# Optimization experiments

Measured on AMD Instinct MI355X. Metric: run time of the kernel, lower is better.

The kernel has to match this reference:

```python
import jax, jax.numpy as jnp
import numpy as np

B, L, D, H, DK, DV = 2, 2048, 512, 8, 64, 64
EPS = 1e-6


def setup_inputs() -> dict:
    key = jax.random.key(0)
    ks = jax.random.split(key, 19)
    n = lambda k, s: jax.random.normal(k, s, dtype=jnp.float32)
    inp = {
        "q_r": n(ks[0], (B, L, D)), "q_i": n(ks[1], (B, L, D)),
        "k_r": n(ks[2], (B, L, D)), "k_i": n(ks[3], (B, L, D)),
        "v_r": n(ks[4], (B, L, D)), "v_i": n(ks[5], (B, L, D)),
        "wq_r": n(ks[6], (D, H * DK)) * 0.02, "wq_i": n(ks[7], (D, H * DK)) * 0.02,
        "wk_r": n(ks[8], (D, H * DK)) * 0.02, "wk_i": n(ks[9], (D, H * DK)) * 0.02,
        "wv_r": n(ks[10], (D, H * DV)) * 0.02, "wv_i": n(ks[11], (D, H * DV)) * 0.02,
        "wo_r": n(ks[12], (H * DV, D)) * 0.02, "wo_i": n(ks[13], (H * DV, D)) * 0.02,
        "ln_wr": n(ks[14], (D,)), "ln_wi": n(ks[15], (D,)),
        "ln_br": n(ks[16], (D,)), "ln_bi": n(ks[17], (D,)),
        "mask": jax.random.randint(ks[18], (B, L, L), 0, 2).astype(jnp.int32),
    }
    return inp


def _clinear(xr, xi, wr, wi):
    # complex matmul (xr + i xi) @ (wr + i wi)
    return xr @ wr - xi @ wi, xi @ wr + xr @ wi


def _complex_layernorm(r, i, wr, wi, br, bi, eps=EPS):
    axes = (1, 2)  # normalize over all non-batch dims of [B, L, D]
    r = r - r.mean(axis=axes, keepdims=True)
    i = i - i.mean(axis=axes, keepdims=True)
    Crr = (r * r).mean(axis=axes, keepdims=True) + eps
    Cii = (i * i).mean(axis=axes, keepdims=True) + eps
    Cri = (r * i).mean(axis=axes, keepdims=True)
    s = jnp.sqrt(Crr * Cii - Cri * Cri)
    t = jnp.sqrt(Crr + Cii + 2.0 * s)
    inv_st = 1.0 / (s * t)
    Rrr = (Cii + s) * inv_st
    Rii = (Crr + s) * inv_st
    Rri = -Cri * inv_st
    nr = Rrr * r + Rri * i
    ni = Rii * i + Rri * r
    # affine: complex multiply by (wr + i wi), then add complex bias
    out_r = nr * wr - ni * wi + br
    out_i = nr * wi + ni * wr + bi
    return out_r, out_i


def reference(q_r, q_i, k_r, k_i, v_r, v_i,
              wq_r, wq_i, wk_r, wk_i, wv_r, wv_i, wo_r, wo_i,
              ln_wr, ln_wi, ln_br, ln_bi, mask):
    res_r, res_i = q_r, q_i
    qr, qi = _clinear(q_r, q_i, wq_r, wq_i)
    kr, ki = _clinear(k_r, k_i, wk_r, wk_i)
    vr, vi = _clinear(v_r, v_i, wv_r, wv_i)
    # [B, L, H*Dk] -> [B, H, L, Dk]
    tohead = lambda x, d: x.reshape(B, L, H, d).transpose(0, 2, 1, 3)
    qr, qi = tohead(qr, DK), tohead(qi, DK)
    kr, ki = tohead(kr, DK), tohead(ki, DK)
    vr, vi = tohead(vr, DV), tohead(vi, DV)
    temp = jnp.float32(DK) ** 0.5
    qr, qi = qr / temp, qi / temp
    # complex scores (q @ conj(k)^T): re + i*im
    sr = jnp.einsum('bhqd,bhkd->bhqk', qr, kr) + jnp.einsum('bhqd,bhkd->bhqk', qi, ki)
    si = jnp.einsum('bhqd,bhkd->bhqk', qi, kr) - jnp.einsum('bhqd,bhkd->bhqk', qr, ki)
    a = jnp.sqrt(sr * sr + si * si)  # abs of complex scores
    a = jnp.where(mask[:, None, :, :] == 0, jnp.float32(-1e9), a)
    attn = jax.nn.softmax(a, axis=-1)  # real-valued attention weights
    out_r = jnp.einsum('bhqk,bhkd->bhqd', attn, vr)
    out_i = jnp.einsum('bhqk,bhkd->bhqd', attn, vi)
    # [B, H, L, Dv] -> [B, L, H*Dv]
    out_r = out_r.transpose(0, 2, 1, 3).reshape(B, L, H * DV)
    out_i = out_i.transpose(0, 2, 1, 3).reshape(B, L, H * DV)
    out_r, out_i = _clinear(out_r, out_i, wo_r, wo_i)
    out_r = out_r + res_r
    out_i = out_i + res_i
    out_r, out_i = _complex_layernorm(out_r, out_i, ln_wr, ln_wi, ln_br, ln_bi)
    return out_r, out_i, attn
```

## Files before the change

kernel.cpp:

```cpp
#include <hip/hip_runtime.h>

typedef unsigned short u16;
typedef unsigned int u32;
typedef unsigned long long u64;


typedef __attribute__((ext_vector_type(8))) short bf16x8;
typedef __attribute__((ext_vector_type(4))) float f32x4;
typedef __attribute__((ext_vector_type(4))) u32 u32x4;

__device__ __forceinline__ u16 f2bf(float f) {
  u32 x = __float_as_uint(f);
  return (u16)((x + 0x7FFFu + ((x >> 16) & 1u)) >> 16);
}
__device__ __forceinline__ u32 pk2(float a, float b) {
  return (u32)f2bf(a) | ((u32)f2bf(b) << 16);
}
__device__ __forceinline__ bf16x8 negv(bf16x8 v) {
  u32x4 x = __builtin_bit_cast(u32x4, v);
  x ^= 0x80008000u;
  return __builtin_bit_cast(bf16x8, x);
}


__global__ __launch_bounds__(256) void pack_a3(
    const float* __restrict__ qr, const float* __restrict__ qi,
    const float* __restrict__ kr, const float* __restrict__ ki,
    const float* __restrict__ vr, const float* __restrict__ vi,
    u16* __restrict__ A) {
  int z = blockIdx.y;
  const float* r  = (z == 0) ? qr : (z == 1) ? kr : vr;
  const float* im = (z == 0) ? qi : (z == 1) ? ki : vi;
  int c = blockIdx.x * 256 + threadIdx.x;
  int m = c >> 7;
  int ck = (c & 127) * 8;
  const float* s = (ck < 512) ? (r + (size_t)m * 512 + ck)
                              : (im + (size_t)m * 512 + (ck - 512));
  float4 a = ((const float4*)s)[0];
  float4 b = ((const float4*)s)[1];
  uint4 o;
  o.x = pk2(a.x, a.y); o.y = pk2(a.z, a.w);
  o.z = pk2(b.x, b.y); o.w = pk2(b.z, b.w);
  ((uint4*)(A + (size_t)z * 4194304))[c] = o;
}

__global__ __launch_bounds__(256) void pack_bt(
    const float* __restrict__ wqr, const float* __restrict__ wqi,
    const float* __restrict__ wkr, const float* __restrict__ wki,
    const float* __restrict__ wvr, const float* __restrict__ wvi,
    const float* __restrict__ wor, const float* __restrict__ woi,
    u16* __restrict__ Btb) {
  int z = blockIdx.y;
  const float* wr = (z==0)?wqr:(z==1)?wkr:(z==2)?wvr:wor;
  const float* wi = (z==0)?wqi:(z==1)?wki:(z==2)?wvi:woi;
  u16* Bt = Btb + (size_t)z * 1048576;
  int n0 = (blockIdx.x >> 4) * 64;
  int k0 = (blockIdx.x & 15) * 64;
  __shared__ float tile[64][65];
  int t = threadIdx.x;
  bool nlow = (n0 < 512), klow = (k0 < 512);
  const float* src = nlow ? (klow ? wr : wi) : (klow ? wi : wr);
  float sgn = (nlow && !klow) ? -1.0f : 1.0f;
  int col0 = nlow ? n0 : n0 - 512;
  int kr0 = klow ? k0 : k0 - 512;
  {
    int rr = t >> 2, cc = (t & 3) * 16;
    const float4* s = (const float4*)(src + (size_t)(kr0 + rr) * 512 + col0 + cc);
#pragma unroll
    for (int j = 0; j < 4; ++j) {
      float4 v = s[j];
      tile[rr][cc + j*4 + 0] = v.x; tile[rr][cc + j*4 + 1] = v.y;
      tile[rr][cc + j*4 + 2] = v.z; tile[rr][cc + j*4 + 3] = v.w;
    }
  }
  __syncthreads();
  {
    int nn = t >> 2, kc = (t & 3) * 16;
    u32 w[8];
#pragma unroll
    for (int j = 0; j < 8; ++j)
      w[j] = pk2(sgn * tile[kc + 2*j][nn], sgn * tile[kc + 2*j + 1][nn]);
    uint4* d = (uint4*)(Bt + (size_t)(n0 + nn) * 1024 + k0 + kc);
    d[0] = make_uint4(w[0], w[1], w[2], w[3]);
    d[1] = make_uint4(w[4], w[5], w[6], w[7]);
  }
}

__global__ __launch_bounds__(256) void pack_mask(const int* __restrict__ mask,
                                                 u64* __restrict__ mb) {
  int tid = blockIdx.x * 256 + threadIdx.x;
  u64 bal = __ballot(mask[tid] != 0);
  if ((threadIdx.x & 63) == 0) mb[tid >> 6] = bal;
}

__global__ __launch_bounds__(256) void pack_vt(const u16* __restrict__ Cvm,
                                               u16* __restrict__ vt) {
  int z = blockIdx.y;
  int b = z >> 3, h = z & 7;
  int lt = blockIdx.x >> 1, ct = blockIdx.x & 1;
  int l0 = lt * 64, c0 = ct * 64;
  int n0 = (ct == 0) ? (h * 64) : (512 + h * 64);
  __shared__ u16 tile[64][80];
  int t = threadIdx.x;
  {
    int lr = t >> 2, cc = (t & 3) * 16;
    const uint4* s = (const uint4*)(Cvm + ((size_t)(b * 2048 + l0 + lr)) * 1024 + n0 + cc);
    uint4 v0 = s[0], v1 = s[1];
    *(uint4*)&tile[lr][cc] = v0;
    *(uint4*)&tile[lr][cc + 8] = v1;
  }
  __syncthreads();
  {
    int cr = t >> 2, lc = (t & 3) * 16;
    u32 w[8];
#pragma unroll
    for (int j = 0; j < 8; ++j)
      w[j] = (u32)tile[lc + 2*j][cr] | ((u32)tile[lc + 2*j + 1][cr] << 16);
    uint4* d = (uint4*)(vt + ((size_t)z * 128 + c0 + cr) * 2048 + l0 + lc);
    d[0] = make_uint4(w[0], w[1], w[2], w[3]);
    d[1] = make_uint4(w[4], w[5], w[6], w[7]);
  }
}


__device__ __forceinline__ void stage_bf(const u16* __restrict__ g, int ld,
                                         u16* lds, int t) {
#pragma unroll
  for (int p = 0; p < 4; ++p) {
    int id = p * 256 + t;
    int r = id >> 3, c = id & 7;
    uint4 v = *(const uint4*)(g + (size_t)r * ld + c * 8);
    *(uint4*)(lds + r * 64 + ((c ^ (r & 7)) << 3)) = v;
  }
}
__device__ __forceinline__ void stage64(const u16* __restrict__ g, int ld,
                                        u16* lds, int t) {
#pragma unroll
  for (int p = 0; p < 2; ++p) {
    int id = p * 256 + t;
    int r = id >> 3, c = id & 7;
    uint4 v = *(const uint4*)(g + (size_t)r * ld + c * 8);
    *(uint4*)(lds + r * 64 + ((c ^ (r & 7)) << 3)) = v;
  }
}

__global__ __launch_bounds__(256) void gemm_proj(const u16* __restrict__ Abase,
                                                 const u16* __restrict__ Btbase,
                                                 u16* __restrict__ Cbase) {
  __shared__ u16 lA[128 * 64], lB[128 * 64];
  int t = threadIdx.x, lane = t & 63, wid = t >> 6;
  int c15 = lane & 15, g = lane >> 4, l7 = lane & 7;
  int z = blockIdx.z;
  const u16* A  = Abase  + (size_t)z * 4194304;
  const u16* Bt = Btbase + (size_t)z * 1048576;
  u16* C = Cbase + (size_t)z * 4194304;
  int brow = blockIdx.y * 128, bcol = blockIdx.x * 128;
  float scale = (z == 0) ? 0.125f : 1.0f;
  int sw0 = ((g ^ l7) << 3), sw1 = (((4 | g) ^ l7) << 3);
  int wr0 = (wid >> 1) * 64 + c15, wc0 = (wid & 1) * 64 + c15;
  const u16 *pA0 = lA + wr0 * 64 + sw0, *pA1 = lA + wr0 * 64 + sw1;
  const u16 *pB0 = lB + wc0 * 64 + sw0, *pB1 = lB + wc0 * 64 + sw1;
  f32x4 zero = {0.f, 0.f, 0.f, 0.f};
  f32x4 acc[4][4];
#pragma unroll
  for (int mi = 0; mi < 4; ++mi)
#pragma unroll
    for (int ni = 0; ni < 4; ++ni) acc[mi][ni] = zero;
  for (int kt = 0; kt < 1024; kt += 64) {
    stage_bf(A + (size_t)brow * 1024 + kt, 1024, lA, t);
    stage_bf(Bt + (size_t)bcol * 1024 + kt, 1024, lB, t);
    __syncthreads();
#pragma unroll
    for (int ks = 0; ks < 2; ++ks) {
      const u16* pa = ks ? pA1 : pA0;
      const u16* pb = ks ? pB1 : pB0;
      bf16x8 fa[4], fb[4];
#pragma unroll
      for (int i2 = 0; i2 < 4; ++i2) {
        fa[i2] = *(const bf16x8*)(pa + i2 * 1024);
        fb[i2] = *(const bf16x8*)(pb + i2 * 1024);
      }
#pragma unroll
      for (int mi = 0; mi < 4; ++mi)
#pragma unroll
        for (int ni = 0; ni < 4; ++ni)
          acc[mi][ni] = __builtin_amdgcn_mfma_f32_16x16x32_bf16(
              fa[mi], fb[ni], acc[mi][ni], 0, 0, 0);
    }
    __syncthreads();
  }
  int wrb = (wid >> 1) * 64, wcb = (wid & 1) * 64;
  int rj = g * 4, cj = c15;
#pragma unroll
  for (int mi = 0; mi < 4; ++mi)
#pragma unroll
    for (int ni = 0; ni < 4; ++ni)
#pragma unroll
      for (int j = 0; j < 4; ++j)
        C[(size_t)(brow + wrb + mi * 16 + rj + j) * 1024 +
          (bcol + wcb + ni * 16 + cj)] = f2bf(acc[mi][ni][j] * scale);
}

__global__ __launch_bounds__(256, 3) void fused_attn(
    const u16* __restrict__ Cq, const u16* __restrict__ Ck,
    const u16* __restrict__ vt, const u64* __restrict__ mb,
    float* __restrict__ attn, u16* __restrict__ Ao) {
  __shared__ u16 lKr[64 * 64], lKi[64 * 64], lV[128 * 64], lP[64 * 64];
  int t = threadIdx.x, lane = t & 63, w = t >> 6;
  int c15 = lane & 15, g = lane >> 4, l7 = lane & 7;
  int strip = blockIdx.x, z = blockIdx.y;
  int b = z >> 3, h = z & 7;
  int q0 = strip * 64;
  int arow = w * 16 + c15;
  int rbase = w * 16 + (g << 2);

  const u16* Qrow = Cq + ((size_t)(b * 2048 + q0 + arow)) * 1024 + h * 64;
  bf16x8 q0r = *(const bf16x8*)(Qrow + g * 8);
  bf16x8 q1r = *(const bf16x8*)(Qrow + 32 + g * 8);
  bf16x8 q0i = *(const bf16x8*)(Qrow + 512 + g * 8);
  bf16x8 q1i = *(const bf16x8*)(Qrow + 544 + g * 8);
  bf16x8 nq0r = negv(q0r), nq1r = negv(q1r);

  int sw0 = ((g ^ l7) << 3), sw1 = (((4 | g) ^ l7) << 3);
  const u16 *pKr0 = lKr + c15 * 64 + sw0, *pKr1 = lKr + c15 * 64 + sw1;
  const u16 *pKi0 = lKi + c15 * 64 + sw0, *pKi1 = lKi + c15 * 64 + sw1;
  const u16 *pV0 = lV + c15 * 64 + sw0, *pV1 = lV + c15 * 64 + sw1;
  const u16 *pP0 = lP + arow * 64 + sw0, *pP1 = lP + arow * 64 + sw1;

  size_t mbase = ((size_t)(b * 2048 + q0 + rbase)) * 32;
  float s[4] = {0.f, 0.f, 0.f, 0.f};
  f32x4 zero = {0.f, 0.f, 0.f, 0.f};
  f32x4 o[8];
#pragma unroll
  for (int ni = 0; ni < 8; ++ni) o[ni] = zero;

  const u16* Kb = Ck + ((size_t)(b * 2048)) * 1024 + h * 64;
  const u16* Vb = vt + (size_t)z * 262144;

  for (int tl = 0; tl < 32; ++tl) {
    int l0 = tl * 64;
    if (tl) __syncthreads();
    stage64(Kb + (size_t)l0 * 1024, 1024, lKr, t);
    stage64(Kb + (size_t)l0 * 1024 + 512, 1024, lKi, t);
    stage_bf(Vb + l0, 2048, lV, t);
    __syncthreads();
    f32x4 sr[4], si[4];
#pragma unroll
    for (int ni = 0; ni < 4; ++ni) { sr[ni] = zero; si[ni] = zero; }
#pragma unroll
    for (int ni = 0; ni < 4; ++ni) {
      bf16x8 g0 = *(const bf16x8*)(pKr0 + ni * 1024);
      bf16x8 g1 = *(const bf16x8*)(pKi0 + ni * 1024);
      sr[ni] = __builtin_amdgcn_mfma_f32_16x16x32_bf16(q0r, g0, sr[ni], 0, 0, 0);
      sr[ni] = __builtin_amdgcn_mfma_f32_16x16x32_bf16(q0i, g1, sr[ni], 0, 0, 0);
      si[ni] = __builtin_amdgcn_mfma_f32_16x16x32_bf16(q0i, g0, si[ni], 0, 0, 0);
      si[ni] = __builtin_amdgcn_mfma_f32_16x16x32_bf16(nq0r, g1, si[ni], 0, 0, 0);
      bf16x8 h0 = *(const bf16x8*)(pKr1 + ni * 1024);
      bf16x8 h1 = *(const bf16x8*)(pKi1 + ni * 1024);
      sr[ni] = __builtin_amdgcn_mfma_f32_16x16x32_bf16(q1r, h0, sr[ni], 0, 0, 0);
      sr[ni] = __builtin_amdgcn_mfma_f32_16x16x32_bf16(q1i, h1, sr[ni], 0, 0, 0);
      si[ni] = __builtin_amdgcn_mfma_f32_16x16x32_bf16(q1i, h0, si[ni], 0, 0, 0);
      si[ni] = __builtin_amdgcn_mfma_f32_16x16x32_bf16(nq1r, h1, si[ni], 0, 0, 0);
    }
    u64 wm[4];
#pragma unroll
    for (int j = 0; j < 4; ++j) wm[j] = mb[mbase + (size_t)j * 32 + tl];
#pragma unroll
    for (int ni = 0; ni < 4; ++ni) {
      int cbit = ni * 16 + c15;
      int pchi = ni * 2 + (c15 >> 3);
#pragma unroll
      for (int j = 0; j < 4; ++j) {
        float n = sr[ni][j] * sr[ni][j] + si[ni][j] * si[ni][j];
        float p = __expf(__builtin_amdgcn_sqrtf(n));
        p = ((wm[j] >> cbit) & 1ull) ? p : 0.0f;
        s[j] += p;
        lP[(rbase + j) * 64 + ((pchi ^ (((g & 1) << 2) + j)) << 3) + l7] = f2bf(p);
      }
    }
    {
      bf16x8 fa0 = *(const bf16x8*)pP0;
      bf16x8 fa1 = *(const bf16x8*)pP1;
#pragma unroll
      for (int ni = 0; ni < 8; ++ni) {
        bf16x8 fb0 = *(const bf16x8*)(pV0 + ni * 1024);
        bf16x8 fb1 = *(const bf16x8*)(pV1 + ni * 1024);
        o[ni] = __builtin_amdgcn_mfma_f32_16x16x32_bf16(fa0, fb0, o[ni], 0, 0, 0);
        o[ni] = __builtin_amdgcn_mfma_f32_16x16x32_bf16(fa1, fb1, o[ni], 0, 0, 0);
      }
    }
  }
  float inv[4];
#pragma unroll
  for (int j = 0; j < 4; ++j) {
    float sj = s[j];
#pragma unroll
    for (int off = 1; off < 16; off <<= 1) sj += __shfl_xor(sj, off);
    inv[j] = 1.0f / sj;
  }
#pragma unroll
  for (int ni = 0; ni < 8; ++ni) {
    int c = ni * 16 + c15;
    int nout = (c < 64) ? (h * 64 + c) : (512 + h * 64 + (c - 64));
#pragma unroll
    for (int j = 0; j < 4; ++j)
      Ao[((size_t)(b * 2048 + q0 + rbase + j)) * 1024 + nout] =
          f2bf(o[ni][j] * inv[j]);
  }
  float* arow_out = attn + ((size_t)z * 2048 + q0 + rbase) * 2048 + c15;
  for (int tl = 0; tl < 32; ++tl) {
    int l0 = tl * 64;
    __syncthreads();
    stage64(Kb + (size_t)l0 * 1024, 1024, lKr, t);
    stage64(Kb + (size_t)l0 * 1024 + 512, 1024, lKi, t);
    __syncthreads();
    f32x4 sr[4], si[4];
#pragma unroll
    for (int ni = 0; ni < 4; ++ni) { sr[ni] = zero; si[ni] = zero; }
#pragma unroll
    for (int ni = 0; ni < 4; ++ni) {
      bf16x8 g0 = *(const bf16x8*)(pKr0 + ni * 1024);
      bf16x8 g1 = *(const bf16x8*)(pKi0 + ni * 1024);
      sr[ni] = __builtin_amdgcn_mfma_f32_16x16x32_bf16(q0r, g0, sr[ni], 0, 0, 0);
      sr[ni] = __builtin_amdgcn_mfma_f32_16x16x32_bf16(q0i, g1, sr[ni], 0, 0, 0);
      si[ni] = __builtin_amdgcn_mfma_f32_16x16x32_bf16(q0i, g0, si[ni], 0, 0, 0);
      si[ni] = __builtin_amdgcn_mfma_f32_16x16x32_bf16(nq0r, g1, si[ni], 0, 0, 0);
      bf16x8 h0 = *(const bf16x8*)(pKr1 + ni * 1024);
      bf16x8 h1 = *(const bf16x8*)(pKi1 + ni * 1024);
      sr[ni] = __builtin_amdgcn_mfma_f32_16x16x32_bf16(q1r, h0, sr[ni], 0, 0, 0);
      sr[ni] = __builtin_amdgcn_mfma_f32_16x16x32_bf16(q1i, h1, sr[ni], 0, 0, 0);
      si[ni] = __builtin_amdgcn_mfma_f32_16x16x32_bf16(q1i, h0, si[ni], 0, 0, 0);
      si[ni] = __builtin_amdgcn_mfma_f32_16x16x32_bf16(nq1r, h1, si[ni], 0, 0, 0);
    }
    u64 wm[4];
#pragma unroll
    for (int j = 0; j < 4; ++j) wm[j] = mb[mbase + (size_t)j * 32 + tl];
    float* outp = arow_out + l0;
#pragma unroll
    for (int ni = 0; ni < 4; ++ni) {
      int cbit = ni * 16 + c15;
#pragma unroll
      for (int j = 0; j < 4; ++j) {
        float n = sr[ni][j] * sr[ni][j] + si[ni][j] * si[ni][j];
        float p = __expf(__builtin_amdgcn_sqrtf(n)) * inv[j];
        p = ((wm[j] >> cbit) & 1ull) ? p : 0.0f;
        outp[(size_t)j * 2048 + ni * 16] = p;
      }
    }
  }
}

__global__ __launch_bounds__(256) void gemm_oproj(
    const u16* __restrict__ A, const u16* __restrict__ Bt,
    const float* __restrict__ resR, const float* __restrict__ resI,
    float* __restrict__ outR, float* __restrict__ outI) {
  __shared__ u16 lA[128 * 64], lB[128 * 64];
  int t = threadIdx.x, lane = t & 63, wid = t >> 6;
  int c15 = lane & 15, g = lane >> 4, l7 = lane & 7;
  int brow = blockIdx.y * 128, bcol = blockIdx.x * 128;
  int sw0 = ((g ^ l7) << 3), sw1 = (((4 | g) ^ l7) << 3);
  int wr0 = (wid >> 1) * 64 + c15, wc0 = (wid & 1) * 64 + c15;
  const u16 *pA0 = lA + wr0 * 64 + sw0, *pA1 = lA + wr0 * 64 + sw1;
  const u16 *pB0 = lB + wc0 * 64 + sw0, *pB1 = lB + wc0 * 64 + sw1;
  f32x4 zero = {0.f, 0.f, 0.f, 0.f};
  f32x4 acc[4][4];
#pragma unroll
  for (int mi = 0; mi < 4; ++mi)
#pragma unroll
    for (int ni = 0; ni < 4; ++ni) acc[mi][ni] = zero;
  for (int kt = 0; kt < 1024; kt += 64) {
    stage_bf(A + (size_t)brow * 1024 + kt, 1024, lA, t);
    stage_bf(Bt + (size_t)bcol * 1024 + kt, 1024, lB, t);
    __syncthreads();
#pragma unroll
    for (int ks = 0; ks < 2; ++ks) {
      const u16* pa = ks ? pA1 : pA0;
      const u16* pb = ks ? pB1 : pB0;
      bf16x8 fa[4], fb[4];
#pragma unroll
      for (int i2 = 0; i2 < 4; ++i2) {
        fa[i2] = *(const bf16x8*)(pa + i2 * 1024);
        fb[i2] = *(const bf16x8*)(pb + i2 * 1024);
      }
#pragma unroll
      for (int mi = 0; mi < 4; ++mi)
#pragma unroll
        for (int ni = 0; ni < 4; ++ni)
          acc[mi][ni] = __builtin_amdgcn_mfma_f32_16x16x32_bf16(
              fa[mi], fb[ni], acc[mi][ni], 0, 0, 0);
    }
    __syncthreads();
  }
  int wrb = (wid >> 1) * 64, wcb = (wid & 1) * 64;
  int rj = g * 4, cj = c15;
#pragma unroll
  for (int mi = 0; mi < 4; ++mi)
#pragma unroll
    for (int ni = 0; ni < 4; ++ni)
#pragma unroll
      for (int j = 0; j < 4; ++j) {
        int row = brow + wrb + mi * 16 + rj + j;
        int col = bcol + wcb + ni * 16 + cj;
        float v = acc[mi][ni][j];
        if (col < 512)
          outR[(size_t)row * 512 + col] = v + resR[(size_t)row * 512 + col];
        else {
          int c2 = col - 512;
          outI[(size_t)row * 512 + c2] = v + resI[(size_t)row * 512 + c2];
        }
      }
}

__global__ __launch_bounds__(256) void ln_reduce(const float* __restrict__ outR,
                                                 const float* __restrict__ outI,
                                                 float* __restrict__ stats) {
  int b = blockIdx.y;
  int t = threadIdx.x;
  size_t base = (size_t)b * 1048576 + (size_t)blockIdx.x * 2048;
  float s0 = 0.f, s1 = 0.f, s2 = 0.f, s3 = 0.f, s4 = 0.f;
#pragma unroll
  for (int p = 0; p < 8; ++p) {
    size_t e = base + p * 256 + t;
    float r = outR[e], i = outI[e];
    s0 += r; s1 += i; s2 += r * r; s3 += i * i; s4 += r * i;
  }
#pragma unroll
  for (int off = 32; off; off >>= 1) {
    s0 += __shfl_xor(s0, off); s1 += __shfl_xor(s1, off);
    s2 += __shfl_xor(s2, off); s3 += __shfl_xor(s3, off);
    s4 += __shfl_xor(s4, off);
  }
  __shared__ float red[4][5];
  if ((t & 63) == 0) {
    int w = t >> 6;
    red[w][0] = s0; red[w][1] = s1; red[w][2] = s2; red[w][3] = s3; red[w][4] = s4;
  }
  __syncthreads();
  if (t == 0) {
    float a0 = red[0][0] + red[1][0] + red[2][0] + red[3][0];
    float a1 = red[0][1] + red[1][1] + red[2][1] + red[3][1];
    float a2 = red[0][2] + red[1][2] + red[2][2] + red[3][2];
    float a3 = red[0][3] + red[1][3] + red[2][3] + red[3][3];
    float a4 = red[0][4] + red[1][4] + red[2][4] + red[3][4];
    atomicAdd(&stats[b * 8 + 0], a0);
    atomicAdd(&stats[b * 8 + 1], a1);
    atomicAdd(&stats[b * 8 + 2], a2);
    atomicAdd(&stats[b * 8 + 3], a3);
    atomicAdd(&stats[b * 8 + 4], a4);
  }
}

__global__ __launch_bounds__(256) void ln_apply(
    float* __restrict__ outR, float* __restrict__ outI,
    const float* __restrict__ stats,
    const float* __restrict__ lnwr, const float* __restrict__ lnwi,
    const float* __restrict__ lnbr, const float* __restrict__ lnbi) {
  int b = blockIdx.y;
  const float* st = stats + b * 8;
  float iN = 1.0f / 1048576.0f;
  float mr = st[0] * iN, mi = st[1] * iN;
  float Crr = st[2] * iN - mr * mr + 1e-6f;
  float Cii = st[3] * iN - mi * mi + 1e-6f;
  float Cri = st[4] * iN - mr * mi;
  float s = sqrtf(fmaxf(Crr * Cii - Cri * Cri, 0.f));
  float tt = sqrtf(Crr + Cii + 2.f * s);
  float inv = 1.0f / (s * tt);
  float Rrr = (Cii + s) * inv, Rii = (Crr + s) * inv, Rri = -Cri * inv;
  size_t e = ((size_t)blockIdx.x * 256 + threadIdx.x) * 4;
  size_t idx = (size_t)b * 1048576 + e;
  int d = (int)(e & 511);
  float4 r4 = *(float4*)(outR + idx);
  float4 i4 = *(float4*)(outI + idx);
  float4 wr = *(const float4*)(lnwr + d);
  float4 wi = *(const float4*)(lnwi + d);
  float4 br = *(const float4*)(lnbr + d);
  float4 bi = *(const float4*)(lnbi + d);
  float4 orr, oii;
#pragma unroll
  for (int j = 0; j < 4; ++j) {
    float r = ((&r4.x)[j]) - mr;
    float i = ((&i4.x)[j]) - mi;
    float nr = Rrr * r + Rri * i;
    float ni = Rii * i + Rri * r;
    (&orr.x)[j] = nr * (&wr.x)[j] - ni * (&wi.x)[j] + (&br.x)[j];
    (&oii.x)[j] = nr * (&wi.x)[j] + ni * (&wr.x)[j] + (&bi.x)[j];
  }
  *(float4*)(outR + idx) = orr;
  *(float4*)(outI + idx) = oii;
}

extern "C" void kernel_launch(void* const* d_in, const int* in_sizes, int n_in,
                              void* d_out, int out_size, void* d_ws, size_t ws_size,
                              hipStream_t stream) {
  const float* q_r = (const float*)d_in[0];
  const float* q_i = (const float*)d_in[1];
  const float* k_r = (const float*)d_in[2];
  const float* k_i = (const float*)d_in[3];
  const float* v_r = (const float*)d_in[4];
  const float* v_i = (const float*)d_in[5];
  const float* wq_r = (const float*)d_in[6];
  const float* wq_i = (const float*)d_in[7];
  const float* wk_r = (const float*)d_in[8];
  const float* wk_i = (const float*)d_in[9];
  const float* wv_r = (const float*)d_in[10];
  const float* wv_i = (const float*)d_in[11];
  const float* wo_r = (const float*)d_in[12];
  const float* wo_i = (const float*)d_in[13];
  const float* ln_wr = (const float*)d_in[14];
  const float* ln_wi = (const float*)d_in[15];
  const float* ln_br = (const float*)d_in[16];
  const float* ln_bi = (const float*)d_in[17];
  const int* mask = (const int*)d_in[18];

  float* outR = (float*)d_out;
  float* outI = outR + 2097152;
  float* attn = outR + 4194304;

  char* ws = (char*)d_ws;
  u16* Aq = (u16*)ws;
  u16* Bt = (u16*)(ws + 25165824);
  u16* Cq = (u16*)(ws + 33554432);
  u16* Ck = Cq + 4194304;
  u16* Cv = Cq + 8388608;
  u16* vt = Aq;
  u16* Ao = (u16*)(ws + 58720256);
  u64* mb = (u64*)(ws + 67108864);
  float* stats = (float*)(ws + 69206016);

  pack_a3<<<dim3(2048, 3), 256, 0, stream>>>(q_r, q_i, k_r, k_i, v_r, v_i, Aq);
  pack_bt<<<dim3(256, 4), 256, 0, stream>>>(wq_r, wq_i, wk_r, wk_i, wv_r, wv_i,
                                            wo_r, wo_i, Bt);
  pack_mask<<<dim3(32768), 256, 0, stream>>>(mask, mb);
  gemm_proj<<<dim3(8, 32, 3), 256, 0, stream>>>(Aq, Bt, Cq);
  pack_vt<<<dim3(64, 16), 256, 0, stream>>>(Cv, vt);
  fused_attn<<<dim3(32, 16), 256, 0, stream>>>(Cq, Ck, vt, mb, attn, Ao);
  gemm_oproj<<<dim3(8, 32), 256, 0, stream>>>(Ao, Bt + 3145728, q_r, q_i, outR, outI);
  hipMemsetAsync(stats, 0, 64, stream);
  ln_reduce<<<dim3(512, 2), 256, 0, stream>>>(outR, outI, stats);
  ln_apply<<<dim3(1024, 2), 256, 0, stream>>>(outR, outI, stats, ln_wr, ln_wi,
                                              ln_br, ln_bi);
}
```

Baseline: 364.9 us.

## Prefetch next tiles into registers and double-buffer LDS in GEMMs and attention

Both GEMM kernels now load the next K-slice into registers while computing on the current LDS tile, then write it to LDS after the compute. The attention kernel double-buffers the K/V LDS tiles in both passes so global loads overlap MFMA work. It also remaps blocks so consecutive blocks share a head and batch, uses nontemporal stores for the attention matrix, and replaces hipMemsetAsync with a tiny zeroing kernel. The cost is more LDS and registers, so attention occupancy is lowered from 3 to 2 blocks per CU.

```diff
diff --git a/kernel.cpp b/kernel.cpp
--- a/kernel.cpp
+++ b/kernel.cpp
@@ -123,24 +123,38 @@
 }
 
 
-__device__ __forceinline__ void stage_bf(const u16* __restrict__ g, int ld,
-                                         u16* lds, int t) {
+__device__ __forceinline__ void ld_t64(const u16* __restrict__ g, int ld, int t,
+                                       uint4 r[2]) {
+#pragma unroll
+  for (int p = 0; p < 2; ++p) {
+    int id = p * 256 + t;
+    int rr = id >> 3, c = id & 7;
+    r[p] = *(const uint4*)(g + (size_t)rr * ld + c * 8);
+  }
+}
+__device__ __forceinline__ void st_t64(u16* lds, int t, const uint4 r[2]) {
+#pragma unroll
+  for (int p = 0; p < 2; ++p) {
+    int id = p * 256 + t;
+    int rr = id >> 3, c = id & 7;
+    *(uint4*)(lds + rr * 64 + ((c ^ (rr & 7)) << 3)) = r[p];
+  }
+}
+__device__ __forceinline__ void ld_t128(const u16* __restrict__ g, int ld, int t,
+                                        uint4 r[4]) {
 #pragma unroll
   for (int p = 0; p < 4; ++p) {
     int id = p * 256 + t;
-    int r = id >> 3, c = id & 7;
-    uint4 v = *(const uint4*)(g + (size_t)r * ld + c * 8);
-    *(uint4*)(lds + r * 64 + ((c ^ (r & 7)) << 3)) = v;
-  }
-}
-__device__ __forceinline__ void stage64(const u16* __restrict__ g, int ld,
-                                        u16* lds, int t) {
-#pragma unroll
-  for (int p = 0; p < 2; ++p) {
+    int rr = id >> 3, c = id & 7;
+    r[p] = *(const uint4*)(g + (size_t)rr * ld + c * 8);
+  }
+}
+__device__ __forceinline__ void st_t128(u16* lds, int t, const uint4 r[4]) {
+#pragma unroll
+  for (int p = 0; p < 4; ++p) {
     int id = p * 256 + t;
-    int r = id >> 3, c = id & 7;
-    uint4 v = *(const uint4*)(g + (size_t)r * ld + c * 8);
-    *(uint4*)(lds + r * 64 + ((c ^ (r & 7)) << 3)) = v;
+    int rr = id >> 3, c = id & 7;
+    *(uint4*)(lds + rr * 64 + ((c ^ (rr & 7)) << 3)) = r[p];
   }
 }
 
@@ -166,10 +180,19 @@
   for (int mi = 0; mi < 4; ++mi)
 #pragma unroll
     for (int ni = 0; ni < 4; ++ni) acc[mi][ni] = zero;
-  for (int kt = 0; kt < 1024; kt += 64) {
-    stage_bf(A + (size_t)brow * 1024 + kt, 1024, lA, t);
-    stage_bf(Bt + (size_t)bcol * 1024 + kt, 1024, lB, t);
+  const u16* Ab = A + (size_t)brow * 1024;
+  const u16* Bb = Bt + (size_t)bcol * 1024;
+  uint4 ra[4], rb[4];
+  ld_t128(Ab, 1024, t, ra);
+  ld_t128(Bb, 1024, t, rb);
+  st_t128(lA, t, ra);
+  st_t128(lB, t, rb);
+  for (int kt = 0; kt < 16; ++kt) {
     __syncthreads();
+    if (kt < 15) {
+      ld_t128(Ab + (kt + 1) * 64, 1024, t, ra);
+      ld_t128(Bb + (kt + 1) * 64, 1024, t, rb);
+    }
 #pragma unroll
     for (int ks = 0; ks < 2; ++ks) {
       const u16* pa = ks ? pA1 : pA0;
@@ -188,6 +211,10 @@
               fa[mi], fb[ni], acc[mi][ni], 0, 0, 0);
     }
     __syncthreads();
+    if (kt < 15) {
+      st_t128(lA, t, ra);
+      st_t128(lB, t, rb);
+    }
   }
   int wrb = (wid >> 1) * 64, wcb = (wid & 1) * 64;
   int rj = g * 4, cj = c15;
@@ -201,14 +228,16 @@
           (bcol + wcb + ni * 16 + cj)] = f2bf(acc[mi][ni][j] * scale);
 }
 
-__global__ __launch_bounds__(256, 3) void fused_attn(
+__global__ __launch_bounds__(256, 2) void fused_attn(
     const u16* __restrict__ Cq, const u16* __restrict__ Ck,
     const u16* __restrict__ vt, const u64* __restrict__ mb,
     float* __restrict__ attn, u16* __restrict__ Ao) {
-  __shared__ u16 lKr[64 * 64], lKi[64 * 64], lV[128 * 64], lP[64 * 64];
+  __shared__ u16 lKr[2][4096], lKi[2][4096], lV[2][8192], lP[4096];
   int t = threadIdx.x, lane = t & 63, w = t >> 6;
   int c15 = lane & 15, g = lane >> 4, l7 = lane & 7;
-  int strip = blockIdx.x, z = blockIdx.y;
+  int f = blockIdx.x + (int)gridDim.x * blockIdx.y;
+  int wk = (f & 7) * 64 + (f >> 3);
+  int strip = wk & 31, z = wk >> 5;
   int b = z >> 3, h = z & 7;
   int q0 = strip * 64;
   int arow = w * 16 + c15;
@@ -222,9 +251,6 @@
   bf16x8 nq0r = negv(q0r), nq1r = negv(q1r);
 
   int sw0 = ((g ^ l7) << 3), sw1 = (((4 | g) ^ l7) << 3);
-  const u16 *pKr0 = lKr + c15 * 64 + sw0, *pKr1 = lKr + c15 * 64 + sw1;
-  const u16 *pKi0 = lKi + c15 * 64 + sw0, *pKi1 = lKi + c15 * 64 + sw1;
-  const u16 *pV0 = lV + c15 * 64 + sw0, *pV1 = lV + c15 * 64 + sw1;
   const u16 *pP0 = lP + arow * 64 + sw0, *pP1 = lP + arow * 64 + sw1;
 
   size_t mbase = ((size_t)(b * 2048 + q0 + rbase)) * 32;
@@ -237,26 +263,39 @@
   const u16* Kb = Ck + ((size_t)(b * 2048)) * 1024 + h * 64;
   const u16* Vb = vt + (size_t)z * 262144;
 
+  uint4 kr[2], ki[2], vv[4];
+  ld_t64(Kb, 1024, t, kr);
+  ld_t64(Kb + 512, 1024, t, ki);
+  ld_t128(Vb, 2048, t, vv);
+  st_t64(lKr[0], t, kr);
+  st_t64(lKi[0], t, ki);
+  st_t128(lV[0], t, vv);
+
   for (int tl = 0; tl < 32; ++tl) {
-    int l0 = tl * 64;
-    if (tl) __syncthreads();
-    stage64(Kb + (size_t)l0 * 1024, 1024, lKr, t);
-    stage64(Kb + (size_t)l0 * 1024 + 512, 1024, lKi, t);
-    stage_bf(Vb + l0, 2048, lV, t);
+    int cur = tl & 1;
     __syncthreads();
+    if (tl < 31) {
+      size_t l1 = (size_t)(tl + 1) * 64;
+      ld_t64(Kb + l1 * 1024, 1024, t, kr);
+      ld_t64(Kb + l1 * 1024 + 512, 1024, t, ki);
+      ld_t128(Vb + l1, 2048, t, vv);
+    }
+    const u16* bKr = lKr[cur] + c15 * 64;
+    const u16* bKi = lKi[cur] + c15 * 64;
+    const u16* bV  = lV[cur] + c15 * 64;
     f32x4 sr[4], si[4];
 #pragma unroll
     for (int ni = 0; ni < 4; ++ni) { sr[ni] = zero; si[ni] = zero; }
 #pragma unroll
     for (int ni = 0; ni < 4; ++ni) {
-      bf16x8 g0 = *(const bf16x8*)(pKr0 + ni * 1024);
-      bf16x8 g1 = *(const bf16x8*)(pKi0 + ni * 1024);
+      bf16x8 g0 = *(const bf16x8*)(bKr + ni * 1024 + sw0);
+      bf16x8 g1 = *(const bf16x8*)(bKi + ni * 1024 + sw0);
       sr[ni] = __builtin_amdgcn_mfma_f32_16x16x32_bf16(q0r, g0, sr[ni], 0, 0, 0);
       sr[ni] = __builtin_amdgcn_mfma_f32_16x16x32_bf16(q0i, g1, sr[ni], 0, 0, 0);
       si[ni] = __builtin_amdgcn_mfma_f32_16x16x32_bf16(q0i, g0, si[ni], 0, 0, 0);
       si[ni] = __builtin_amdgcn_mfma_f32_16x16x32_bf16(nq0r, g1, si[ni], 0, 0, 0);
-      bf16x8 h0 = *(const bf16x8*)(pKr1 + ni * 1024);
-      bf16x8 h1 = *(const bf16x8*)(pKi1 + ni * 1024);
+      bf16x8 h0 = *(const bf16x8*)(bKr + ni * 1024 + sw1);
+      bf16x8 h1 = *(const bf16x8*)(bKi + ni * 1024 + sw1);
       sr[ni] = __builtin_amdgcn_mfma_f32_16x16x32_bf16(q1r, h0, sr[ni], 0, 0, 0);
       sr[ni] = __builtin_amdgcn_mfma_f32_16x16x32_bf16(q1i, h1, sr[ni], 0, 0, 0);
       si[ni] = __builtin_amdgcn_mfma_f32_16x16x32_bf16(q1i, h0, si[ni], 0, 0, 0);
@@ -283,12 +322,17 @@
       bf16x8 fa1 = *(const bf16x8*)pP1;
 #pragma unroll
       for (int ni = 0; ni < 8; ++ni) {
-        bf16x8 fb0 = *(const bf16x8*)(pV0 + ni * 1024);
-        bf16x8 fb1 = *(const bf16x8*)(pV1 + ni * 1024);
+        bf16x8 fb0 = *(const bf16x8*)(bV + ni * 1024 + sw0);
+        bf16x8 fb1 = *(const bf16x8*)(bV + ni * 1024 + sw1);
         o[ni] = __builtin_amdgcn_mfma_f32_16x16x32_bf16(fa0, fb0, o[ni], 0, 0, 0);
         o[ni] = __builtin_amdgcn_mfma_f32_16x16x32_bf16(fa1, fb1, o[ni], 0, 0, 0);
       }
     }
+    if (tl < 31) {
+      st_t64(lKr[cur ^ 1], t, kr);
+      st_t64(lKi[cur ^ 1], t, ki);
+      st_t128(lV[cur ^ 1], t, vv);
+    }
   }
   float inv[4];
 #pragma unroll
@@ -308,25 +352,35 @@
           f2bf(o[ni][j] * inv[j]);
   }
   float* arow_out = attn + ((size_t)z * 2048 + q0 + rbase) * 2048 + c15;
+  ld_t64(Kb, 1024, t, kr);
+  ld_t64(Kb + 512, 1024, t, ki);
+  __syncthreads();
+  st_t64(lKr[0], t, kr);
+  st_t64(lKi[0], t, ki);
   for (int tl = 0; tl < 32; ++tl) {
+    int cur = tl & 1;
     int l0 = tl * 64;
     __syncthreads();
-    stage64(Kb + (size_t)l0 * 1024, 1024, lKr, t);
-    stage64(Kb + (size_t)l0 * 1024 + 512, 1024, lKi, t);
-    __syncthreads();
+    if (tl < 31) {
+      size_t l1 = (size_t)(tl + 1) * 64;
+      ld_t64(Kb + l1 * 1024, 1024, t, kr);
+      ld_t64(Kb + l1 * 1024 + 512, 1024, t, ki);
+    }
+    const u16* bKr = lKr[cur] + c15 * 64;
+    const u16* bKi = lKi[cur] + c15 * 64;
     f32x4 sr[4], si[4];
 #pragma unroll
     for (int ni = 0; ni < 4; ++ni) { sr[ni] = zero; si[ni] = zero; }
 #pragma unroll
     for (int ni = 0; ni < 4; ++ni) {
-      bf16x8 g0 = *(const bf16x8*)(pKr0 + ni * 1024);
-      bf16x8 g1 = *(const bf16x8*)(pKi0 + ni * 1024);
+      bf16x8 g0 = *(const bf16x8*)(bKr + ni * 1024 + sw0);
+      bf16x8 g1 = *(const bf16x8*)(bKi + ni * 1024 + sw0);
       sr[ni] = __builtin_amdgcn_mfma_f32_16x16x32_bf16(q0r, g0, sr[ni], 0, 0, 0);
       sr[ni] = __builtin_amdgcn_mfma_f32_16x16x32_bf16(q0i, g1, sr[ni], 0, 0, 0);
       si[ni] = __builtin_amdgcn_mfma_f32_16x16x32_bf16(q0i, g0, si[ni], 0, 0, 0);
       si[ni] = __builtin_amdgcn_mfma_f32_16x16x32_bf16(nq0r, g1, si[ni], 0, 0, 0);
-      bf16x8 h0 = *(const bf16x8*)(pKr1 + ni * 1024);
-      bf16x8 h1 = *(const bf16x8*)(pKi1 + ni * 1024);
+      bf16x8 h0 = *(const bf16x8*)(bKr + ni * 1024 + sw1);
+      bf16x8 h1 = *(const bf16x8*)(bKi + ni * 1024 + sw1);
       sr[ni] = __builtin_amdgcn_mfma_f32_16x16x32_bf16(q1r, h0, sr[ni], 0, 0, 0);
       sr[ni] = __builtin_amdgcn_mfma_f32_16x16x32_bf16(q1i, h1, sr[ni], 0, 0, 0);
       si[ni] = __builtin_amdgcn_mfma_f32_16x16x32_bf16(q1i, h0, si[ni], 0, 0, 0);
@@ -344,8 +398,12 @@
         float n = sr[ni][j] * sr[ni][j] + si[ni][j] * si[ni][j];
         float p = __expf(__builtin_amdgcn_sqrtf(n)) * inv[j];
         p = ((wm[j] >> cbit) & 1ull) ? p : 0.0f;
-        outp[(size_t)j * 2048 + ni * 16] = p;
+        __builtin_nontemporal_store(p, outp + (size_t)j * 2048 + ni * 16);
       }
+    }
+    if (tl < 31) {
+      st_t64(lKr[cur ^ 1], t, kr);
+      st_t64(lKi[cur ^ 1], t, ki);
     }
   }
 }
@@ -368,10 +426,19 @@
   for (int mi = 0; mi < 4; ++mi)
 #pragma unroll
     for (int ni = 0; ni < 4; ++ni) acc[mi][ni] = zero;
-  for (int kt = 0; kt < 1024; kt += 64) {
-    stage_bf(A + (size_t)brow * 1024 + kt, 1024, lA, t);
-    stage_bf(Bt + (size_t)bcol * 1024 + kt, 1024, lB, t);
+  const u16* Ab = A + (size_t)brow * 1024;
+  const u16* Bb = Bt + (size_t)bcol * 1024;
+  uint4 ra[4], rb[4];
+  ld_t128(Ab, 1024, t, ra);
+  ld_t128(Bb, 1024, t, rb);
+  st_t128(lA, t, ra);
+  st_t128(lB, t, rb);
+  for (int kt = 0; kt < 16; ++kt) {
     __syncthreads();
+    if (kt < 15) {
+      ld_t128(Ab + (kt + 1) * 64, 1024, t, ra);
+      ld_t128(Bb + (kt + 1) * 64, 1024, t, rb);
+    }
 #pragma unroll
     for (int ks = 0; ks < 2; ++ks) {
       const u16* pa = ks ? pA1 : pA0;
@@ -390,6 +457,10 @@
               fa[mi], fb[ni], acc[mi][ni], 0, 0, 0);
     }
     __syncthreads();
+    if (kt < 15) {
+      st_t128(lA, t, ra);
+      st_t128(lB, t, rb);
+    }
   }
   int wrb = (wid >> 1) * 64, wcb = (wid & 1) * 64;
   int rj = g * 4, cj = c15;
@@ -409,6 +480,10 @@
           outI[(size_t)row * 512 + c2] = v + resI[(size_t)row * 512 + c2];
         }
       }
+}
+
+__global__ void zero_stats(float* __restrict__ stats) {
+  if (threadIdx.x < 16) stats[threadIdx.x] = 0.0f;
 }
 
 __global__ __launch_bounds__(256) void ln_reduce(const float* __restrict__ outR,
@@ -531,11 +606,11 @@
   pack_bt<<<dim3(256, 4), 256, 0, stream>>>(wq_r, wq_i, wk_r, wk_i, wv_r, wv_i,
                                             wo_r, wo_i, Bt);
   pack_mask<<<dim3(32768), 256, 0, stream>>>(mask, mb);
+  zero_stats<<<dim3(1), 64, 0, stream>>>(stats);
   gemm_proj<<<dim3(8, 32, 3), 256, 0, stream>>>(Aq, Bt, Cq);
   pack_vt<<<dim3(64, 16), 256, 0, stream>>>(Cv, vt);
   fused_attn<<<dim3(32, 16), 256, 0, stream>>>(Cq, Ck, vt, mb, attn, Ao);
   gemm_oproj<<<dim3(8, 32), 256, 0, stream>>>(Ao, Bt + 3145728, q_r, q_i, outR, outI);
-  hipMemsetAsync(stats, 0, 64, stream);
   ln_reduce<<<dim3(512, 2), 256, 0, stream>>>(outR, outI, stats);
   ln_apply<<<dim3(1024, 2), 256, 0, stream>>>(outR, outI, stats, ln_wr, ln_wi,
                                               ln_br, ln_bi);
```

New measurement: 498.5 us. +36.6%, slower.
